# Kernel tuning notes

Hardware: AMD Instinct MI355X
Metric: run time of the kernel (lower is better)

Reference implementation:

```python
import jax, jax.numpy as jnp
import numpy as np

B, N, D_IN, D_OUT = 4, 2048, 1024, 1024

def setup_inputs() -> dict:
    key = jax.random.key(0)
    ks = jax.random.split(key, 7)
    s_in = 1.0 / np.sqrt(D_IN)
    return {
        "X": jax.random.normal(ks[0], (B, N, D_IN), dtype=jnp.float32),
        "Wq": jax.random.uniform(ks[1], (D_IN, D_OUT), jnp.float32, -s_in, s_in),
        "bq": jax.random.uniform(ks[2], (D_OUT,), jnp.float32, -s_in, s_in),
        "Wk": jax.random.uniform(ks[3], (D_IN, D_OUT), jnp.float32, -s_in, s_in),
        "bk": jax.random.uniform(ks[4], (D_OUT,), jnp.float32, -s_in, s_in),
        "Wv": jax.random.uniform(ks[5], (D_IN, D_OUT), jnp.float32, -s_in, s_in),
        "bv": jax.random.uniform(ks[6], (D_OUT,), jnp.float32, -s_in, s_in),
    }

def reference(X, Wq, bq, Wk, bk, Wv, bv):
    # QKV projections: [B,N,D_in] @ [D_in,D_out] -> [B,N,D_out]
    q = jnp.einsum('bnd,de->bne', X, Wq) + bq
    k = jnp.einsum('bnd,de->bne', X, Wk) + bk
    v = jnp.einsum('bnd,de->bne', X, Wv) + bv
    # Unscaled attention (faithful: original has no 1/sqrt(d))
    scores = jnp.einsum('bne,bme->bnm', q, k)  # [B,N,N]
    weights = jax.nn.softmax(scores, axis=-1)
    return jnp.einsum('bnm,bme->bne', weights, v)
```

## Files before the change

kernel.cpp:

```cpp
#include <hip/hip_runtime.h>
#include <hip/hip_bf16.h>
#include <hip/hip_fp16.h>
#include <stdint.h>
#include <math.h>


typedef unsigned short ushort_t;
typedef __attribute__((ext_vector_type(8))) _Float16  f16x8;
typedef __attribute__((ext_vector_type(4))) _Float16  f16x4;
typedef __attribute__((ext_vector_type(4))) float     f32x4;

__device__ __forceinline__ void async_load16(const void* g, void* l) {
  __builtin_amdgcn_global_load_lds(
      (const __attribute__((address_space(1))) void*)g,
      (__attribute__((address_space(3))) void*)l, 16, 0, 0);
}

__global__ __launch_bounds__(256)
void qkv_gemm_kernel(const ushort_t* __restrict__ A, const ushort_t* __restrict__ BT,
                     const float* __restrict__ bq, const float* __restrict__ bk,
                     const float* __restrict__ bvp,
                     __half* __restrict__ Qh, __half* __restrict__ Kh,
                     ushort_t* __restrict__ Vt)
{
  const int K = 1024;
  __shared__ ushort_t As[2][128 * 32];
  __shared__ ushort_t Bs[2][128 * 32];

  const int t    = threadIdx.x;
  const int lane = t & 63;
  const int wave = t >> 6;
  const int wm   = (wave >> 1) * 64;
  const int wn   = (wave & 1) * 64;

  const ushort_t* Ab = A + (long)blockIdx.y * 128 * K;
  const ushort_t* Bb = BT + (long)blockIdx.x * 128 * K;

  const int ldr = t >> 2;
  const int swzs = (ldr & 3) ^ ((ldr >> 2) & 3);
  const int ldc = ((t & 3) ^ swzs) * 8;
  const int frow = lane & 15;
  const int fsz  = (frow & 3) ^ ((frow >> 2) & 3);
  const int fo   = (((lane >> 4) ^ fsz)) * 8;

  f32x4 acc[4][4];
  const f32x4 zero = {0.0f, 0.0f, 0.0f, 0.0f};
#pragma unroll
  for (int i = 0; i < 4; ++i)
#pragma unroll
    for (int j = 0; j < 4; ++j) acc[i][j] = zero;

  for (int k0 = 0; k0 < K; k0 += 64) {
    __syncthreads();
    const ushort_t* ga = Ab + (long)ldr * K + k0 + ldc;
    const ushort_t* gb = Bb + (long)ldr * K + k0 + ldc;
#pragma unroll
    for (int h = 0; h < 2; ++h) {
      async_load16(ga + h * 32,                &As[h][t * 8]);
      async_load16(ga + h * 32 + 64 * (long)K, &As[h][2048 + t * 8]);
      async_load16(gb + h * 32,                &Bs[h][t * 8]);
      async_load16(gb + h * 32 + 64 * (long)K, &Bs[h][2048 + t * 8]);
    }
    __syncthreads();
#pragma unroll
    for (int h = 0; h < 2; ++h) {
      f16x8 af[4], bf[4];
#pragma unroll
      for (int i = 0; i < 4; ++i) {
        af[i] = *(const f16x8*)&As[h][(wm + i * 16 + frow) * 32 + fo];
        bf[i] = *(const f16x8*)&Bs[h][(wn + i * 16 + frow) * 32 + fo];
      }
#pragma unroll
      for (int mi = 0; mi < 4; ++mi)
#pragma unroll
        for (int ni = 0; ni < 4; ++ni)
          acc[mi][ni] = __builtin_amdgcn_mfma_f32_16x16x32_f16(af[mi], bf[ni], acc[mi][ni], 0, 0, 0);
    }
  }

  const int er = (lane >> 4) * 4;
  const int ec = lane & 15;
  const int tgt = blockIdx.x >> 3;
  const float* bias = (tgt == 0) ? bq : (tgt == 1) ? bk : bvp;
#pragma unroll
  for (int ni = 0; ni < 4; ++ni) {
    const int c = (blockIdx.x & 7) * 128 + wn + ni * 16 + ec;
    const float bval = bias[c];
#pragma unroll
    for (int mi = 0; mi < 4; ++mi) {
      const long grow0 = (long)blockIdx.y * 128 + wm + mi * 16 + er;
      if (tgt < 2) {
        __half* o = (tgt == 0) ? Qh : Kh;
#pragma unroll
        for (int r = 0; r < 4; ++r)
          o[(grow0 + r) * 1024 + c] = __float2half(acc[mi][ni][r] + bval);
      } else {
        const long b  = grow0 >> 11;
        const long ml = grow0 & 2047;
        f16x4 v4;
#pragma unroll
        for (int r = 0; r < 4; ++r) v4[r] = (_Float16)(acc[mi][ni][r] + bval);
        *(f16x4*)&Vt[b * 2097152 + (long)c * 2048 + ml] = v4;
      }
    }
  }
}

__global__ __launch_bounds__(256)
void qk_gemm_kernel(const ushort_t* __restrict__ Q, const ushort_t* __restrict__ Kh,
                    __half* __restrict__ S, float* __restrict__ PM, float* __restrict__ PS)
{
  const int K = 1024;
  __shared__ ushort_t As[2][128 * 32];
  __shared__ ushort_t Bs[2][128 * 32];

  const int t    = threadIdx.x;
  const int lane = t & 63;
  const int wave = t >> 6;
  const int wm   = (wave >> 1) * 64;
  const int wn   = (wave & 1) * 64;
  const long z   = blockIdx.z;

  const ushort_t* Ab = Q + z * 2048 * 1024 + (long)blockIdx.y * 128 * K;
  const ushort_t* Bb = Kh + z * 2048 * 1024 + (long)blockIdx.x * 128 * K;
  __half* Sb = S + z * 2048 * 2048;

  const int ldr = t >> 2;
  const int swzs = (ldr & 3) ^ ((ldr >> 2) & 3);
  const int ldc = ((t & 3) ^ swzs) * 8;
  const int frow = lane & 15;
  const int fsz  = (frow & 3) ^ ((frow >> 2) & 3);
  const int fo   = (((lane >> 4) ^ fsz)) * 8;

  f32x4 acc[4][4];
  const f32x4 zero = {0.0f, 0.0f, 0.0f, 0.0f};
#pragma unroll
  for (int i = 0; i < 4; ++i)
#pragma unroll
    for (int j = 0; j < 4; ++j) acc[i][j] = zero;

  for (int k0 = 0; k0 < K; k0 += 64) {
    __syncthreads();
    const ushort_t* ga = Ab + (long)ldr * K + k0 + ldc;
    const ushort_t* gb = Bb + (long)ldr * K + k0 + ldc;
#pragma unroll
    for (int h = 0; h < 2; ++h) {
      async_load16(ga + h * 32,                &As[h][t * 8]);
      async_load16(ga + h * 32 + 64 * (long)K, &As[h][2048 + t * 8]);
      async_load16(gb + h * 32,                &Bs[h][t * 8]);
      async_load16(gb + h * 32 + 64 * (long)K, &Bs[h][2048 + t * 8]);
    }
    __syncthreads();
#pragma unroll
    for (int h = 0; h < 2; ++h) {
      f16x8 af[4], bf[4];
#pragma unroll
      for (int i = 0; i < 4; ++i) {
        af[i] = *(const f16x8*)&As[h][(wm + i * 16 + frow) * 32 + fo];
        bf[i] = *(const f16x8*)&Bs[h][(wn + i * 16 + frow) * 32 + fo];
      }
#pragma unroll
      for (int mi = 0; mi < 4; ++mi)
#pragma unroll
        for (int ni = 0; ni < 4; ++ni)
          acc[mi][ni] = __builtin_amdgcn_mfma_f32_16x16x32_f16(af[mi], bf[ni], acc[mi][ni], 0, 0, 0);
    }
  }

  const int er = (lane >> 4) * 4;
  const int ec = lane & 15;
  const int cc = blockIdx.x * 2 + (wave & 1);
  float* PMb = PM + z * 32 * 2048 + (long)cc * 2048;
  float* PSb = PS + z * 32 * 2048 + (long)cc * 2048;

#pragma unroll
  for (int mi = 0; mi < 4; ++mi)
#pragma unroll
    for (int r = 0; r < 4; ++r) {
      float m = fmaxf(fmaxf(acc[mi][0][r], acc[mi][1][r]),
                      fmaxf(acc[mi][2][r], acc[mi][3][r]));
      m = fmaxf(m, __shfl_xor(m, 1));
      m = fmaxf(m, __shfl_xor(m, 2));
      m = fmaxf(m, __shfl_xor(m, 4));
      m = fmaxf(m, __shfl_xor(m, 8));
      float s = 0.0f;
#pragma unroll
      for (int ni = 0; ni < 4; ++ni) {
        const float e = __expf(acc[mi][ni][r] - m);
        acc[mi][ni][r] = e;
        s += e;
      }
      s += __shfl_xor(s, 1);
      s += __shfl_xor(s, 2);
      s += __shfl_xor(s, 4);
      s += __shfl_xor(s, 8);
      if (ec == 0) {
        const long row = (long)blockIdx.y * 128 + wm + mi * 16 + er + r;
        PMb[row] = m;
        PSb[row] = s;
      }
    }

#pragma unroll
  for (int ni = 0; ni < 4; ++ni) {
    const long col = (long)blockIdx.x * 128 + wn + ni * 16 + ec;
#pragma unroll
    for (int mi = 0; mi < 4; ++mi)
#pragma unroll
      for (int r = 0; r < 4; ++r) {
        const long grow = (long)blockIdx.y * 128 + wm + mi * 16 + er + r;
        Sb[grow * 2048 + col] = __float2half(acc[mi][ni][r]);
      }
  }
}

__global__ __launch_bounds__(256)
void softmax_reduce_kernel(const float* __restrict__ PM, const float* __restrict__ PS,
                           float* __restrict__ Sc)
{
  const int r = blockIdx.x * 256 + threadIdx.x;
  const int b = r >> 11, row = r & 2047;
  const long base = (long)b * 32 * 2048 + row;
  float m = -3.4e38f;
#pragma unroll
  for (int cb = 0; cb < 32; ++cb) m = fmaxf(m, PM[base + cb * 2048]);
  float l = 0.0f;
#pragma unroll
  for (int cb = 0; cb < 32; ++cb) l += PS[base + cb * 2048] * __expf(PM[base + cb * 2048] - m);
  const float inv = 1.0f / l;
#pragma unroll
  for (int cb = 0; cb < 32; ++cb) Sc[base + cb * 2048] = __expf(PM[base + cb * 2048] - m) * inv;
}

__global__ __launch_bounds__(256)
void pv_gemm_kernel(const ushort_t* __restrict__ S, const ushort_t* __restrict__ Vt,
                    const float* __restrict__ Sc, float* __restrict__ Out)
{
  const int K = 2048;
  __shared__ ushort_t As[2][128 * 32];
  __shared__ ushort_t Bs[2][128 * 32];

  const int t    = threadIdx.x;
  const int lane = t & 63;
  const int wave = t >> 6;
  const int wm   = (wave >> 1) * 64;
  const int wn   = (wave & 1) * 64;
  const long z   = blockIdx.z;

  const ushort_t* Ab = S + z * 2048 * 2048 + (long)blockIdx.y * 128 * K;
  const ushort_t* Bb = Vt + z * 1024 * 2048 + (long)blockIdx.x * 128 * K;
  const float* Scb = Sc + z * 32 * 2048;
  float* Cb = Out + z * 2048 * 1024;

  const int ldr = t >> 2;
  const int swzs = (ldr & 3) ^ ((ldr >> 2) & 3);
  const int ldc = ((t & 3) ^ swzs) * 8;
  const int frow = lane & 15;
  const int fsz  = (frow & 3) ^ ((frow >> 2) & 3);
  const int fo   = (((lane >> 4) ^ fsz)) * 8;

  const int arow0 = blockIdx.y * 128 + wm + frow;

  f32x4 acc[4][4];
  const f32x4 zero = {0.0f, 0.0f, 0.0f, 0.0f};
#pragma unroll
  for (int i = 0; i < 4; ++i)
#pragma unroll
    for (int j = 0; j < 4; ++j) acc[i][j] = zero;

  for (int k0 = 0; k0 < K; k0 += 64) {
    const int cb = k0 >> 6;
    _Float16 sc16[4];
#pragma unroll
    for (int i = 0; i < 4; ++i)
      sc16[i] = (_Float16)Scb[(long)cb * 2048 + arow0 + i * 16];

    __syncthreads();
    const ushort_t* ga = Ab + (long)ldr * K + k0 + ldc;
    const ushort_t* gb = Bb + (long)ldr * K + k0 + ldc;
#pragma unroll
    for (int h = 0; h < 2; ++h) {
      async_load16(ga + h * 32,                &As[h][t * 8]);
      async_load16(ga + h * 32 + 64 * (long)K, &As[h][2048 + t * 8]);
      async_load16(gb + h * 32,                &Bs[h][t * 8]);
      async_load16(gb + h * 32 + 64 * (long)K, &Bs[h][2048 + t * 8]);
    }
    __syncthreads();
#pragma unroll
    for (int h = 0; h < 2; ++h) {
      f16x8 af[4], bf[4];
#pragma unroll
      for (int i = 0; i < 4; ++i) {
        af[i] = *(const f16x8*)&As[h][(wm + i * 16 + frow) * 32 + fo] * sc16[i];
        bf[i] = *(const f16x8*)&Bs[h][(wn + i * 16 + frow) * 32 + fo];
      }
#pragma unroll
      for (int mi = 0; mi < 4; ++mi)
#pragma unroll
        for (int ni = 0; ni < 4; ++ni)
          acc[mi][ni] = __builtin_amdgcn_mfma_f32_16x16x32_f16(af[mi], bf[ni], acc[mi][ni], 0, 0, 0);
    }
  }

  const int er = (lane >> 4) * 4;
  const int ec = lane & 15;
#pragma unroll
  for (int ni = 0; ni < 4; ++ni) {
    const int gcol = blockIdx.x * 128 + wn + ni * 16 + ec;
#pragma unroll
    for (int mi = 0; mi < 4; ++mi) {
#pragma unroll
      for (int r = 0; r < 4; ++r) {
        const long grow = (long)blockIdx.y * 128 + wm + mi * 16 + er + r;
        Cb[grow * 1024 + gcol] = acc[mi][ni][r];
      }
    }
  }
}

__global__ __launch_bounds__(256)
void cvt_f32_f16_kernel(const float* __restrict__ src, __half* __restrict__ dst, long n)
{
  const long i = ((long)blockIdx.x * 256 + threadIdx.x) * 8;
  if (i + 8 > n) return;
  const float4 a = *(const float4*)(src + i);
  const float4 b = *(const float4*)(src + i + 4);
  f16x8 h;
  h[0] = (_Float16)a.x; h[1] = (_Float16)a.y; h[2] = (_Float16)a.z; h[3] = (_Float16)a.w;
  h[4] = (_Float16)b.x; h[5] = (_Float16)b.y; h[6] = (_Float16)b.z; h[7] = (_Float16)b.w;
  *(f16x8*)((ushort_t*)dst + i) = h;
}

__global__ __launch_bounds__(256)
void transpose_cvt3_kernel(const float* __restrict__ W0, const float* __restrict__ W1,
                           const float* __restrict__ W2, __half* __restrict__ dst)
{
  __shared__ float tile[32][33];
  const int z = blockIdx.z;
  const float* src = (z == 0) ? W0 : (z == 1) ? W1 : W2;
  __half* d = dst + (long)z * 1024 * 1024;
  const int c0 = blockIdx.x * 32;
  const int r0 = blockIdx.y * 32;
  const int tx = threadIdx.x & 31;
  const int ty = threadIdx.x >> 5;
#pragma unroll
  for (int i = 0; i < 32; i += 8)
    tile[ty + i][tx] = src[(long)(r0 + ty + i) * 1024 + (c0 + tx)];
  __syncthreads();
#pragma unroll
  for (int i = 0; i < 32; i += 8)
    d[(long)(c0 + ty + i) * 1024 + (r0 + tx)] = __float2half(tile[tx][ty + i]);
}

extern "C" void kernel_launch(void* const* d_in, const int* in_sizes, int n_in,
                              void* d_out, int out_size, void* d_ws, size_t ws_size,
                              hipStream_t stream)
{
  const int  Bb = 4, Nn = 2048, Dd = 1024;
  const long BN = (long)Bb * Nn;

  const float* X  = (const float*)d_in[0];
  const float* Wq = (const float*)d_in[1];
  const float* bq = (const float*)d_in[2];
  const float* Wk = (const float*)d_in[3];
  const float* bk = (const float*)d_in[4];
  const float* Wv = (const float*)d_in[5];
  const float* bv = (const float*)d_in[6];
  float* Out      = (float*)d_out;

  uint8_t* w = (uint8_t*)d_ws;
  ushort_t* Wt = (ushort_t*)w;  w += (size_t)3 * Dd * Dd * 2;

  transpose_cvt3_kernel<<<dim3(Dd / 32, Dd / 32, 3), 256, 0, stream>>>(Wq, Wk, Wv, (__half*)Wt);

  const size_t statsBytes = (size_t)Bb * 32 * Nn * 4;
  const size_t fullNeed = (size_t)3 * Dd * Dd * 2
                        + 4 * ((size_t)BN * Dd * 2)
                        + (size_t)Bb * Nn * Nn * 2
                        + 3 * statsBytes;

  if (ws_size >= fullNeed) {
    ushort_t* Xh = (ushort_t*)w;  w += (size_t)BN * Dd * 2;
    ushort_t* Q  = (ushort_t*)w;  w += (size_t)BN * Dd * 2;
    ushort_t* Kb = (ushort_t*)w;  w += (size_t)BN * Dd * 2;
    ushort_t* Vt = (ushort_t*)w;  w += (size_t)BN * Dd * 2;
    ushort_t* S  = (ushort_t*)w;  w += (size_t)Bb * Nn * Nn * 2;
    float*    PM = (float*)w;     w += statsBytes;
    float*    PS = (float*)w;     w += statsBytes;
    float*    Sc = (float*)w;

    cvt_f32_f16_kernel<<<dim3((unsigned)(BN * Dd / (8 * 256))), 256, 0, stream>>>(
        X, (__half*)Xh, BN * Dd);

    qkv_gemm_kernel<<<dim3(3 * Dd / 128, BN / 128, 1), 256, 0, stream>>>(
        Xh, Wt, bq, bk, bv, (__half*)Q, (__half*)Kb, Vt);

    qk_gemm_kernel<<<dim3(Nn / 128, Nn / 128, Bb), 256, 0, stream>>>(
        Q, Kb, (__half*)S, PM, PS);

    softmax_reduce_kernel<<<dim3((unsigned)(Bb * Nn / 256)), 256, 0, stream>>>(PM, PS, Sc);

    pv_gemm_kernel<<<dim3(Dd / 128, Nn / 128, Bb), 256, 0, stream>>>(
        S, Vt, Sc, Out);
  } else {
    ushort_t* Xh = (ushort_t*)w;  w += (size_t)Nn * Dd * 2;
    ushort_t* Q  = (ushort_t*)w;  w += (size_t)Nn * Dd * 2;
    ushort_t* Kb = (ushort_t*)w;  w += (size_t)Nn * Dd * 2;
    ushort_t* Vt = (ushort_t*)w;  w += (size_t)Nn * Dd * 2;
    ushort_t* S  = (ushort_t*)w;  w += (size_t)Nn * Nn * 2;
    float*    PM = (float*)w;     w += (size_t)32 * Nn * 4;
    float*    PS = (float*)w;     w += (size_t)32 * Nn * 4;
    float*    Sc = (float*)w;

    for (int b = 0; b < Bb; ++b) {
      const float* Xb = X + (long)b * Nn * Dd;
      cvt_f32_f16_kernel<<<dim3((unsigned)((long)Nn * Dd / (8 * 256))), 256, 0, stream>>>(
          Xb, (__half*)Xh, (long)Nn * Dd);
      qkv_gemm_kernel<<<dim3(3 * Dd / 128, Nn / 128, 1), 256, 0, stream>>>(
          Xh, Wt, bq, bk, bv, (__half*)Q, (__half*)Kb, Vt);
      qk_gemm_kernel<<<dim3(Nn / 128, Nn / 128, 1), 256, 0, stream>>>(
          Q, Kb, (__half*)S, PM, PS);
      softmax_reduce_kernel<<<dim3((unsigned)(Nn / 256)), 256, 0, stream>>>(PM, PS, Sc);
      pv_gemm_kernel<<<dim3(Dd / 128, Nn / 128, 1), 256, 0, stream>>>(
          S, Vt, Sc, Out + (long)b * Nn * Dd);
    }
  }
}
```

Measured before the change: 274.6 us.

## Use 256x256 tiles with pipelined async LDS staging for QKV and QK GEMMs

Replaces the 128x128 single-buffer GEMM mainloop in the QKV projection and QK^T kernels with a 256x256-tile, 8-wave kernel. It double-buffers 64-wide K slices in 128KB of LDS, interleaves async global-to-LDS loads with MFMA quarters, and separates them with explicit barriers, s_setprio and partial vmcnt waits. A grouped block-id remap is added to improve L2 reuse. The goal is higher arithmetic intensity and overlap of global loads with compute. In exchange it uses much more LDS per block, raises register pressure with 32 accumulators per thread, and gives fewer blocks per grid for the tail.

```diff
diff --git a/kernel.cpp b/kernel.cpp
--- a/kernel.cpp
+++ b/kernel.cpp
@@ -16,178 +16,232 @@
       (__attribute__((address_space(3))) void*)l, 16, 0, 0);
 }
 
-__global__ __launch_bounds__(256)
-void qkv_gemm_kernel(const ushort_t* __restrict__ A, const ushort_t* __restrict__ BT,
-                     const float* __restrict__ bq, const float* __restrict__ bk,
-                     const float* __restrict__ bvp,
-                     __half* __restrict__ Qh, __half* __restrict__ Kh,
-                     ushort_t* __restrict__ Vt)
-{
-  const int K = 1024;
-  __shared__ ushort_t As[2][128 * 32];
-  __shared__ ushort_t Bs[2][128 * 32];
-
+#define A0OFF 0
+#define B0OFF 16384
+#define A1OFF 32768
+#define B1OFF 49152
+
+template<int SHIFT>
+__device__ __forceinline__ void stage_half(const ushort_t* __restrict__ gb,
+                                           int k0, int q, ushort_t* lt, int t)
+{
+#pragma unroll
+  for (int j = 0; j < 2; ++j) {
+    const int i   = j * 64 + (t >> 3);
+    const int row = ((i >> SHIFT) << (SHIFT + 1)) | (q << SHIFT) | (i & ((1 << SHIFT) - 1));
+    const int ch  = (t & 7) ^ (row & 7);
+    async_load16(gb + (long)row * 1024 + k0 + ch * 8, lt + row * 64 + (t & 7) * 8);
+  }
+}
+
+#define BARR do { __builtin_amdgcn_sched_barrier(0); \
+                  __builtin_amdgcn_s_barrier();      \
+                  __builtin_amdgcn_sched_barrier(0); } while (0)
+
+#define RD_A(TP, QM)                                                          \
+  do { _Pragma("unroll") for (int m_ = 0; m_ < 4; ++m_) {                     \
+    af[m_][0] = *(const f16x8*)&(TP)[(arow0 + (QM)*64 + m_*16) * 64 + ck0];   \
+    af[m_][1] = *(const f16x8*)&(TP)[(arow0 + (QM)*64 + m_*16) * 64 + ck1];   \
+  } } while (0)
+
+#define RD_B(TP, QN)                                                          \
+  do { _Pragma("unroll") for (int n_ = 0; n_ < 2; ++n_) {                     \
+    bf[n_][0] = *(const f16x8*)&(TP)[(brow0 + (QN)*32 + n_*16) * 64 + ck0];   \
+    bf[n_][1] = *(const f16x8*)&(TP)[(brow0 + (QN)*32 + n_*16) * 64 + ck1];   \
+  } } while (0)
+
+#define MM(QM, QN)                                                            \
+  do { __builtin_amdgcn_s_setprio(1);                                         \
+  _Pragma("unroll") for (int kh_ = 0; kh_ < 2; ++kh_)                         \
+    _Pragma("unroll") for (int m_ = 0; m_ < 4; ++m_)                          \
+      _Pragma("unroll") for (int n_ = 0; n_ < 2; ++n_)                        \
+        acc[(QM)*4+m_][(QN)*2+n_] = __builtin_amdgcn_mfma_f32_16x16x32_f16(   \
+            af[m_][kh_], bf[n_][kh_], acc[(QM)*4+m_][(QN)*2+n_], 0, 0, 0);    \
+  __builtin_amdgcn_s_setprio(0); } while (0)
+
+template<bool LAST>
+__device__ __forceinline__ void iter256(const ushort_t* __restrict__ Ab,
+                                        const ushort_t* __restrict__ Bb,
+                                        ushort_t* lds, f32x4 (&acc)[8][4],
+                                        int ka, int t, int arow0, int brow0,
+                                        int ck0, int ck1)
+{
+  const int kb = ka + 64, kc = ka + 128, kd = ka + 192;
+  f16x8 af[4][2], bf[2][2];
+
+  RD_A(lds + A0OFF, 0); RD_B(lds + B0OFF, 0);
+  stage_half<5>(Bb, kb, 0, lds + B1OFF, t);
+  BARR; MM(0, 0); BARR;
+
+  RD_B(lds + B0OFF, 1);
+  if constexpr (!LAST) stage_half<6>(Ab, kc, 0, lds + A0OFF, t);
+  BARR; MM(0, 1); BARR;
+
+  RD_A(lds + A0OFF, 1);
+  if constexpr (!LAST) stage_half<5>(Bb, kc, 1, lds + B0OFF, t);
+  BARR; MM(1, 1); BARR;
+
+  RD_B(lds + B0OFF, 0);
+  if constexpr (!LAST) stage_half<6>(Ab, kc, 1, lds + A0OFF, t);
+  BARR; MM(1, 0);
+  if constexpr (LAST) asm volatile("s_waitcnt vmcnt(0)" ::: "memory");
+  else                asm volatile("s_waitcnt vmcnt(6)" ::: "memory");
+  BARR;
+
+  RD_A(lds + A1OFF, 0); RD_B(lds + B1OFF, 0);
+  if constexpr (!LAST) stage_half<5>(Bb, kc, 0, lds + B0OFF, t);
+  BARR; MM(0, 0); BARR;
+
+  RD_B(lds + B1OFF, 1);
+  if constexpr (!LAST) stage_half<6>(Ab, kd, 0, lds + A1OFF, t);
+  BARR; MM(0, 1); BARR;
+
+  RD_A(lds + A1OFF, 1);
+  if constexpr (!LAST) stage_half<5>(Bb, kd, 1, lds + B1OFF, t);
+  BARR; MM(1, 1); BARR;
+
+  RD_B(lds + B1OFF, 0);
+  if constexpr (!LAST) stage_half<6>(Ab, kd, 1, lds + A1OFF, t);
+  BARR; MM(1, 0);
+  if constexpr (!LAST) asm volatile("s_waitcnt vmcnt(6)" ::: "memory");
+  BARR;
+}
+
+__device__ __forceinline__ void gemm256(const ushort_t* __restrict__ Ab,
+                                        const ushort_t* __restrict__ Bb,
+                                        ushort_t* lds, f32x4 (&acc)[8][4])
+{
   const int t    = threadIdx.x;
   const int lane = t & 63;
   const int wave = t >> 6;
-  const int wm   = (wave >> 1) * 64;
-  const int wn   = (wave & 1) * 64;
-
-  const ushort_t* Ab = A + (long)blockIdx.y * 128 * K;
-  const ushort_t* Bb = BT + (long)blockIdx.x * 128 * K;
-
-  const int ldr = t >> 2;
-  const int swzs = (ldr & 3) ^ ((ldr >> 2) & 3);
-  const int ldc = ((t & 3) ^ swzs) * 8;
-  const int frow = lane & 15;
-  const int fsz  = (frow & 3) ^ ((frow >> 2) & 3);
-  const int fo   = (((lane >> 4) ^ fsz)) * 8;
-
-  f32x4 acc[4][4];
+  const int wr   = wave >> 2;
+  const int wc   = wave & 3;
+  const int arow0 = wr * 128 + (lane & 15);
+  const int brow0 = wc * 64  + (lane & 15);
+  const int ck0 = (((lane >> 4)    ) ^ (lane & 7)) * 8;
+  const int ck1 = ((4 + (lane >> 4)) ^ (lane & 7)) * 8;
+
+  stage_half<6>(Ab,  0, 0, lds + A0OFF, t);
+  stage_half<5>(Bb,  0, 1, lds + B0OFF, t);
+  stage_half<6>(Ab,  0, 1, lds + A0OFF, t);
+  stage_half<5>(Bb,  0, 0, lds + B0OFF, t);
+  stage_half<6>(Ab, 64, 0, lds + A1OFF, t);
+  stage_half<5>(Bb, 64, 1, lds + B1OFF, t);
+  stage_half<6>(Ab, 64, 1, lds + A1OFF, t);
+  asm volatile("s_waitcnt vmcnt(6)" ::: "memory");
+  BARR;
+
+#pragma unroll 1
+  for (int it = 0; it < 7; ++it)
+    iter256<false>(Ab, Bb, lds, acc, it * 128, t, arow0, brow0, ck0, ck1);
+  iter256<true>(Ab, Bb, lds, acc, 896, t, arow0, brow0, ck0, ck1);
+}
+
+__global__ __launch_bounds__(512, 2)
+void qkv256_kernel(const ushort_t* __restrict__ A, const ushort_t* __restrict__ BT,
+                   const float* __restrict__ bq, const float* __restrict__ bk,
+                   const float* __restrict__ bvp,
+                   __half* __restrict__ Qh, __half* __restrict__ Kh,
+                   ushort_t* __restrict__ Vt)
+{
+  __shared__ __align__(16) ushort_t lds[65536];
+
+  const int nb = gridDim.x * gridDim.y;
+  int id = blockIdx.y * gridDim.x + blockIdx.x;
+  id = (id & 7) * (nb >> 3) + (id >> 3);
+  const int bx = id % gridDim.x;
+  const int by = id / gridDim.x;
+
+  const ushort_t* Ab = A  + (long)by * 256 * 1024;
+  const ushort_t* Bb = BT + (long)bx * 256 * 1024;
+
+  f32x4 acc[8][4];
   const f32x4 zero = {0.0f, 0.0f, 0.0f, 0.0f};
 #pragma unroll
-  for (int i = 0; i < 4; ++i)
+  for (int i = 0; i < 8; ++i)
 #pragma unroll
     for (int j = 0; j < 4; ++j) acc[i][j] = zero;
 
-  for (int k0 = 0; k0 < K; k0 += 64) {
-    __syncthreads();
-    const ushort_t* ga = Ab + (long)ldr * K + k0 + ldc;
-    const ushort_t* gb = Bb + (long)ldr * K + k0 + ldc;
-#pragma unroll
-    for (int h = 0; h < 2; ++h) {
-      async_load16(ga + h * 32,                &As[h][t * 8]);
-      async_load16(ga + h * 32 + 64 * (long)K, &As[h][2048 + t * 8]);
-      async_load16(gb + h * 32,                &Bs[h][t * 8]);
-      async_load16(gb + h * 32 + 64 * (long)K, &Bs[h][2048 + t * 8]);
-    }
-    __syncthreads();
-#pragma unroll
-    for (int h = 0; h < 2; ++h) {
-      f16x8 af[4], bf[4];
-#pragma unroll
-      for (int i = 0; i < 4; ++i) {
-        af[i] = *(const f16x8*)&As[h][(wm + i * 16 + frow) * 32 + fo];
-        bf[i] = *(const f16x8*)&Bs[h][(wn + i * 16 + frow) * 32 + fo];
-      }
-#pragma unroll
-      for (int mi = 0; mi < 4; ++mi)
-#pragma unroll
-        for (int ni = 0; ni < 4; ++ni)
-          acc[mi][ni] = __builtin_amdgcn_mfma_f32_16x16x32_f16(af[mi], bf[ni], acc[mi][ni], 0, 0, 0);
-    }
-  }
-
-  const int er = (lane >> 4) * 4;
-  const int ec = lane & 15;
-  const int tgt = blockIdx.x >> 3;
+  gemm256(Ab, Bb, lds, acc);
+
+  const int t = threadIdx.x, lane = t & 63, wave = t >> 6;
+  const int wr = wave >> 2, wc = wave & 3;
+  const int er = (lane >> 4) * 4, ec = lane & 15;
+  const int tgt = bx >> 2;
   const float* bias = (tgt == 0) ? bq : (tgt == 1) ? bk : bvp;
-#pragma unroll
-  for (int ni = 0; ni < 4; ++ni) {
-    const int c = (blockIdx.x & 7) * 128 + wn + ni * 16 + ec;
-    const float bval = bias[c];
-#pragma unroll
-    for (int mi = 0; mi < 4; ++mi) {
-      const long grow0 = (long)blockIdx.y * 128 + wm + mi * 16 + er;
+
+#pragma unroll
+  for (int n4 = 0; n4 < 4; ++n4) {
+    const int col = (bx & 3) * 256 + wc * 64 + n4 * 16 + ec;
+    const float bval = bias[col];
+#pragma unroll
+    for (int m8 = 0; m8 < 8; ++m8) {
+      const long grow0 = (long)by * 256 + wr * 128 + m8 * 16 + er;
       if (tgt < 2) {
         __half* o = (tgt == 0) ? Qh : Kh;
 #pragma unroll
         for (int r = 0; r < 4; ++r)
-          o[(grow0 + r) * 1024 + c] = __float2half(acc[mi][ni][r] + bval);
+          o[(grow0 + r) * 1024 + col] = __float2half(acc[m8][n4][r] + bval);
       } else {
         const long b  = grow0 >> 11;
         const long ml = grow0 & 2047;
         f16x4 v4;
 #pragma unroll
-        for (int r = 0; r < 4; ++r) v4[r] = (_Float16)(acc[mi][ni][r] + bval);
-        *(f16x4*)&Vt[b * 2097152 + (long)c * 2048 + ml] = v4;
-      }
-    }
-  }
-}
-
-__global__ __launch_bounds__(256)
-void qk_gemm_kernel(const ushort_t* __restrict__ Q, const ushort_t* __restrict__ Kh,
-                    __half* __restrict__ S, float* __restrict__ PM, float* __restrict__ PS)
-{
-  const int K = 1024;
-  __shared__ ushort_t As[2][128 * 32];
-  __shared__ ushort_t Bs[2][128 * 32];
-
-  const int t    = threadIdx.x;
-  const int lane = t & 63;
-  const int wave = t >> 6;
-  const int wm   = (wave >> 1) * 64;
-  const int wn   = (wave & 1) * 64;
-  const long z   = blockIdx.z;
-
-  const ushort_t* Ab = Q + z * 2048 * 1024 + (long)blockIdx.y * 128 * K;
-  const ushort_t* Bb = Kh + z * 2048 * 1024 + (long)blockIdx.x * 128 * K;
+        for (int r = 0; r < 4; ++r) v4[r] = (_Float16)(acc[m8][n4][r] + bval);
+        *(f16x4*)&Vt[b * 2097152 + (long)col * 2048 + ml] = v4;
+      }
+    }
+  }
+}
+
+__global__ __launch_bounds__(512, 2)
+void qk256_kernel(const ushort_t* __restrict__ Q, const ushort_t* __restrict__ Kh,
+                  __half* __restrict__ S, float* __restrict__ PM, float* __restrict__ PS)
+{
+  __shared__ __align__(16) ushort_t lds[65536];
+
+  const int nb = gridDim.x * gridDim.y;
+  int id = blockIdx.y * gridDim.x + blockIdx.x;
+  id = (id & 7) * (nb >> 3) + (id >> 3);
+  const int bx = id % gridDim.x;
+  const int by = id / gridDim.x;
+  const long z = blockIdx.z;
+
+  const ushort_t* Ab = Q  + z * 2048 * 1024 + (long)by * 256 * 1024;
+  const ushort_t* Bb = Kh + z * 2048 * 1024 + (long)bx * 256 * 1024;
   __half* Sb = S + z * 2048 * 2048;
 
-  const int ldr = t >> 2;
-  const int swzs = (ldr & 3) ^ ((ldr >> 2) & 3);
-  const int ldc = ((t & 3) ^ swzs) * 8;
-  const int frow = lane & 15;
-  const int fsz  = (frow & 3) ^ ((frow >> 2) & 3);
-  const int fo   = (((lane >> 4) ^ fsz)) * 8;
-
-  f32x4 acc[4][4];
+  f32x4 acc[8][4];
   const f32x4 zero = {0.0f, 0.0f, 0.0f, 0.0f};
 #pragma unroll
-  for (int i = 0; i < 4; ++i)
+  for (int i = 0; i < 8; ++i)
 #pragma unroll
     for (int j = 0; j < 4; ++j) acc[i][j] = zero;
 
-  for (int k0 = 0; k0 < K; k0 += 64) {
-    __syncthreads();
-    const ushort_t* ga = Ab + (long)ldr * K + k0 + ldc;
-    const ushort_t* gb = Bb + (long)ldr * K + k0 + ldc;
-#pragma unroll
-    for (int h = 0; h < 2; ++h) {
-      async_load16(ga + h * 32,                &As[h][t * 8]);
-      async_load16(ga + h * 32 + 64 * (long)K, &As[h][2048 + t * 8]);
-      async_load16(gb + h * 32,                &Bs[h][t * 8]);
-      async_load16(gb + h * 32 + 64 * (long)K, &Bs[h][2048 + t * 8]);
-    }
-    __syncthreads();
-#pragma unroll
-    for (int h = 0; h < 2; ++h) {
-      f16x8 af[4], bf[4];
-#pragma unroll
-      for (int i = 0; i < 4; ++i) {
-        af[i] = *(const f16x8*)&As[h][(wm + i * 16 + frow) * 32 + fo];
-        bf[i] = *(const f16x8*)&Bs[h][(wn + i * 16 + frow) * 32 + fo];
-      }
-#pragma unroll
-      for (int mi = 0; mi < 4; ++mi)
-#pragma unroll
-        for (int ni = 0; ni < 4; ++ni)
-          acc[mi][ni] = __builtin_amdgcn_mfma_f32_16x16x32_f16(af[mi], bf[ni], acc[mi][ni], 0, 0, 0);
-    }
-  }
-
-  const int er = (lane >> 4) * 4;
-  const int ec = lane & 15;
-  const int cc = blockIdx.x * 2 + (wave & 1);
+  gemm256(Ab, Bb, lds, acc);
+
+  const int t = threadIdx.x, lane = t & 63, wave = t >> 6;
+  const int wr = wave >> 2, wc = wave & 3;
+  const int er = (lane >> 4) * 4, ec = lane & 15;
+  const int cc = bx * 4 + wc;
   float* PMb = PM + z * 32 * 2048 + (long)cc * 2048;
   float* PSb = PS + z * 32 * 2048 + (long)cc * 2048;
 
 #pragma unroll
-  for (int mi = 0; mi < 4; ++mi)
+  for (int m8 = 0; m8 < 8; ++m8)
 #pragma unroll
     for (int r = 0; r < 4; ++r) {
-      float m = fmaxf(fmaxf(acc[mi][0][r], acc[mi][1][r]),
-                      fmaxf(acc[mi][2][r], acc[mi][3][r]));
+      float m = fmaxf(fmaxf(acc[m8][0][r], acc[m8][1][r]),
+                      fmaxf(acc[m8][2][r], acc[m8][3][r]));
       m = fmaxf(m, __shfl_xor(m, 1));
       m = fmaxf(m, __shfl_xor(m, 2));
       m = fmaxf(m, __shfl_xor(m, 4));
       m = fmaxf(m, __shfl_xor(m, 8));
       float s = 0.0f;
 #pragma unroll
-      for (int ni = 0; ni < 4; ++ni) {
-        const float e = __expf(acc[mi][ni][r] - m);
-        acc[mi][ni][r] = e;
+      for (int n4 = 0; n4 < 4; ++n4) {
+        const float e = __expf(acc[m8][n4][r] - m);
+        acc[m8][n4][r] = e;
         s += e;
       }
       s += __shfl_xor(s, 1);
@@ -195,21 +249,21 @@
       s += __shfl_xor(s, 4);
       s += __shfl_xor(s, 8);
       if (ec == 0) {
-        const long row = (long)blockIdx.y * 128 + wm + mi * 16 + er + r;
+        const long row = (long)by * 256 + wr * 128 + m8 * 16 + er + r;
         PMb[row] = m;
         PSb[row] = s;
       }
     }
 
 #pragma unroll
-  for (int ni = 0; ni < 4; ++ni) {
-    const long col = (long)blockIdx.x * 128 + wn + ni * 16 + ec;
-#pragma unroll
-    for (int mi = 0; mi < 4; ++mi)
+  for (int n4 = 0; n4 < 4; ++n4) {
+    const long col = (long)bx * 256 + wc * 64 + n4 * 16 + ec;
+#pragma unroll
+    for (int m8 = 0; m8 < 8; ++m8)
 #pragma unroll
       for (int r = 0; r < 4; ++r) {
-        const long grow = (long)blockIdx.y * 128 + wm + mi * 16 + er + r;
-        Sb[grow * 2048 + col] = __float2half(acc[mi][ni][r]);
+        const long grow = (long)by * 256 + wr * 128 + m8 * 16 + er + r;
+        Sb[grow * 2048 + col] = __float2half(acc[m8][n4][r]);
       }
   }
 }
@@ -392,10 +446,10 @@
     cvt_f32_f16_kernel<<<dim3((unsigned)(BN * Dd / (8 * 256))), 256, 0, stream>>>(
         X, (__half*)Xh, BN * Dd);
 
-    qkv_gemm_kernel<<<dim3(3 * Dd / 128, BN / 128, 1), 256, 0, stream>>>(
+    qkv256_kernel<<<dim3(3 * Dd / 256, BN / 256, 1), 512, 0, stream>>>(
         Xh, Wt, bq, bk, bv, (__half*)Q, (__half*)Kb, Vt);
 
-    qk_gemm_kernel<<<dim3(Nn / 128, Nn / 128, Bb), 256, 0, stream>>>(
+    qk256_kernel<<<dim3(Nn / 256, Nn / 256, Bb), 512, 0, stream>>>(
         Q, Kb, (__half*)S, PM, PS);
 
     softmax_reduce_kernel<<<dim3((unsigned)(Bb * Nn / 256)), 256, 0, stream>>>(PM, PS, Sc);
@@ -416,9 +470,9 @@
       const float* Xb = X + (long)b * Nn * Dd;
       cvt_f32_f16_kernel<<<dim3((unsigned)((long)Nn * Dd / (8 * 256))), 256, 0, stream>>>(
           Xb, (__half*)Xh, (long)Nn * Dd);
-      qkv_gemm_kernel<<<dim3(3 * Dd / 128, Nn / 128, 1), 256, 0, stream>>>(
+      qkv256_kernel<<<dim3(3 * Dd / 256, Nn / 256, 1), 512, 0, stream>>>(
           Xh, Wt, bq, bk, bv, (__half*)Q, (__half*)Kb, Vt);
-      qk_gemm_kernel<<<dim3(Nn / 128, Nn / 128, 1), 256, 0, stream>>>(
+      qk256_kernel<<<dim3(Nn / 256, Nn / 256, 1), 512, 0, stream>>>(
           Q, Kb, (__half*)S, PM, PS);
       softmax_reduce_kernel<<<dim3((unsigned)(Nn / 256)), 256, 0, stream>>>(PM, PS, Sc);
       pv_gemm_kernel<<<dim3(Dd / 128, Nn / 128, 1), 256, 0, stream>>>(
```

New measurement: 275.2 us. Within noise of the previous version (+0.2%).
